# Kernel tuning notes

Hardware: AMD Instinct MI355X
Metric: run time of the kernel (lower is better)

Reference implementation:

```python
import jax, jax.numpy as jnp
import numpy as np

B, S, HID = 4, 4096, 1024
NUM_HEADS, HEAD_DIM = 16, 64  # HID // NUM_HEADS
EPS = 1e-8  # torch F.cosine_similarity eps


def setup_inputs() -> dict:
    key = jax.random.key(0)
    ks = jax.random.split(key, 12)
    scale = 1.0 / np.sqrt(HID)
    d = {
        "query": jax.random.normal(ks[0], (B, S, HID), jnp.float32),
        "key": jax.random.normal(ks[1], (B, S, HID), jnp.float32),
        "value": jax.random.normal(ks[2], (B, S, HID), jnp.float32),
        "Wq": jax.random.normal(ks[3], (HID, HID), jnp.float32) * scale,
        "bq": jnp.zeros((HID,), jnp.float32),
        "Wk": jax.random.normal(ks[4], (HID, HID), jnp.float32) * scale,
        "bk": jnp.zeros((HID,), jnp.float32),
        "Wv": jax.random.normal(ks[5], (HID, HID), jnp.float32) * scale,
        "bv": jnp.zeros((HID,), jnp.float32),
        "Wo": jax.random.normal(ks[6], (HID, HID), jnp.float32) * scale,
        "bo": jnp.zeros((HID,), jnp.float32),
        "score_weights": jax.random.normal(ks[7], (3,), jnp.float32),
    }
    return d


def reference(query, key, value, Wq, bq, Wk, bk, Wv, bv, Wo, bo, score_weights):
    # Projections; NOTE: original reshapes to (B, S, H, D) and never transposes,
    # so all attention scores are over the HEADS axis (shape (B,S,H,H)).
    q = (query @ Wq + bq).reshape(B, S, NUM_HEADS, HEAD_DIM)
    k = (key @ Wk + bk).reshape(B, S, NUM_HEADS, HEAD_DIM)
    v = (value @ Wv + bv).reshape(B, S, NUM_HEADS, HEAD_DIM)

    # Shared inner products between heads at each (b, s): (B, S, H, H)
    qk = jnp.einsum('bsqd,bskd->bsqk', q, k)

    # 1) scaled dot product
    dot = qk / jnp.sqrt(jnp.float32(HEAD_DIM))

    # 2) cosine similarity (F.cosine_similarity with eps=1e-8)
    qn = jnp.linalg.norm(q, axis=-1)  # (B,S,H)
    kn = jnp.linalg.norm(k, axis=-1)
    cos = qk / jnp.maximum(qn[..., :, None] * kn[..., None, :], EPS)

    # 3) negative Euclidean distance (torch.cdist, p=2)
    sq = jnp.sum(q * q, axis=-1)  # (B,S,H)
    sk = jnp.sum(k * k, axis=-1)
    dist2 = jnp.maximum(sq[..., :, None] + sk[..., None, :] - 2.0 * qk, 0.0)
    dist = -jnp.sqrt(dist2)

    w = jax.nn.softmax(score_weights)
    scores = w[0] * dot + w[1] * cos + w[2] * dist  # (B,S,H,H)

    attention = jax.nn.softmax(scores, axis=-1)  # dropout = identity (eval)
    out = jnp.einsum('bsqk,bskd->bsqd', attention, v)  # (B,S,H,D)

    # Faithful to torch: transpose(1,2) -> (B,H,S,D), then view (B, S, HID)
    out = out.transpose(0, 2, 1, 3).reshape(B, S, HID)
    return out @ Wo + bo, attention
```

## Files before the change

### kernel.cpp

```cpp
#include <hip/hip_runtime.h>
#include <stdint.h>

#define BB 4
#define SS 4096
#define HID 1024
#define NH 16
#define HD 64
#define TOKENS (BB * SS)

typedef unsigned short u16;
typedef __bf16 bf16x8 __attribute__((ext_vector_type(8)));
typedef float f32x4 __attribute__((ext_vector_type(4)));
typedef __attribute__((address_space(1))) unsigned int u32g;
typedef __attribute__((address_space(3))) unsigned int u32l;

__device__ __forceinline__ u16 f2bf(float f) {
  union { float f; unsigned u; } v; v.f = f;
  unsigned u = v.u;
  unsigned r = u + 0x7fffu + ((u >> 16) & 1u);
  return (u16)(r >> 16);
}
__device__ __forceinline__ float bf2f(u16 h) {
  union { unsigned u; float f; } v; v.u = ((unsigned)h) << 16;
  return v.f;
}

__device__ __forceinline__ void async16(const void* g, void* l) {
  __builtin_amdgcn_global_load_lds((const u32g*)g, (u32l*)l, 16, 0, 0);
}

__global__ __launch_bounds__(256) void transpose_cast(
    const float* __restrict__ W, u16* __restrict__ Wt) {
  __shared__ float t[32][33];
  const int bx = blockIdx.x * 32;
  const int by = blockIdx.y * 32;
  const int x = threadIdx.x;
#pragma unroll
  for (int yy = threadIdx.y; yy < 32; yy += 8)
    t[yy][x] = W[(size_t)(by + yy) * HID + bx + x];
  __syncthreads();
#pragma unroll
  for (int yy = threadIdx.y; yy < 32; yy += 8)
    Wt[(size_t)(bx + yy) * HID + by + x] = f2bf(t[x][yy]);
}

template <bool A_BF16, bool C_BF16>
__global__ __launch_bounds__(256, 2) void gemm_bt(
    const void* __restrict__ Av, const u16* __restrict__ Bt,
    const float* __restrict__ bias, void* __restrict__ Cv, int M, int N, int K) {
  __shared__ u16 As[128 * 32];
  __shared__ u16 Bs[128 * 32];
  const int tid = threadIdx.x;
  const int wave = tid >> 6, lane = tid & 63;
  const int quad = lane >> 4, l16 = lane & 15;
  const int m0 = blockIdx.y * 128, n0 = blockIdx.x * 128;
  const int wm = (wave >> 1) * 64, wn = (wave & 1) * 64;

  f32x4 acc[4][4] = {};

  for (int kt = 0; kt < K; kt += 32) {
    __syncthreads();
    {
      const u16* src = Bt + (size_t)n0 * K + kt;
#pragma unroll
      for (int is = 0; is < 2; ++is) {
        int g = is * 256 + wave * 64 + lane;
        const u16* gp = src + (size_t)(g >> 2) * K + (g & 3) * 8;
        u16* lp = &Bs[(is * 256 + wave * 64) * 8];
        async16(gp, lp);
      }
    }
    if (A_BF16) {
      const u16* src = (const u16*)Av + (size_t)m0 * K + kt;
#pragma unroll
      for (int is = 0; is < 2; ++is) {
        int g = is * 256 + wave * 64 + lane;
        const u16* gp = src + (size_t)(g >> 2) * K + (g & 3) * 8;
        u16* lp = &As[(is * 256 + wave * 64) * 8];
        async16(gp, lp);
      }
    } else {
      const float* src = (const float*)Av + (size_t)m0 * K + kt;
#pragma unroll
      for (int c = 0; c < 4; ++c) {
        int g = c * 256 + tid;
        int row = g >> 3, col = (g & 7) * 4;
        float4 f = *(const float4*)(src + (size_t)row * K + col);
        ushort4 h;
        h.x = f2bf(f.x); h.y = f2bf(f.y); h.z = f2bf(f.z); h.w = f2bf(f.w);
        *(ushort4*)&As[row * 32 + col] = h;
      }
    }
    __syncthreads();
    bf16x8 af[4], bfr[4];
#pragma unroll
    for (int i = 0; i < 4; ++i)
      af[i] = *(const bf16x8*)&As[(wm + i * 16 + l16) * 32 + quad * 8];
#pragma unroll
    for (int j = 0; j < 4; ++j)
      bfr[j] = *(const bf16x8*)&Bs[(wn + j * 16 + l16) * 32 + quad * 8];
#pragma unroll
    for (int i = 0; i < 4; ++i)
#pragma unroll
      for (int j = 0; j < 4; ++j)
        acc[i][j] = __builtin_amdgcn_mfma_f32_16x16x32_bf16(af[i], bfr[j],
                                                            acc[i][j], 0, 0, 0);
  }

  const int cb = n0 + wn + l16;
#pragma unroll
  for (int i = 0; i < 4; ++i) {
    int rowb = m0 + wm + i * 16 + quad * 4;
#pragma unroll
    for (int j = 0; j < 4; ++j) {
      int col = cb + j * 16;
      float bv = bias[col];
#pragma unroll
      for (int r = 0; r < 4; ++r) {
        float v = acc[i][j][r] + bv;
        if (C_BF16)
          ((u16*)Cv)[(size_t)(rowb + r) * N + col] = f2bf(v);
        else
          ((float*)Cv)[(size_t)(rowb + r) * N + col] = v;
      }
    }
  }
}

__global__ __launch_bounds__(256, 4) void attention_kernel(
    const u16* __restrict__ qb, const u16* __restrict__ kb,
    const u16* __restrict__ vb, const float* __restrict__ sw,
    float* __restrict__ attn_out, u16* __restrict__ o) {
  __shared__ float qs[16][65], ks[16][65], vs[16][65];
  __shared__ float sq[16], sk[16], qn[16], kn[16];
  __shared__ float attn_s[16][17];
  const int tid = threadIdx.x;
  const int token = blockIdx.x;
  const size_t base = (size_t)token * HID;

  {
    int idx = tid * 4;
    int h = idx >> 6, d = idx & 63;
    ushort4 uq = *(const ushort4*)(qb + base + idx);
    ushort4 uk = *(const ushort4*)(kb + base + idx);
    ushort4 uv = *(const ushort4*)(vb + base + idx);
    qs[h][d] = bf2f(uq.x); qs[h][d + 1] = bf2f(uq.y);
    qs[h][d + 2] = bf2f(uq.z); qs[h][d + 3] = bf2f(uq.w);
    ks[h][d] = bf2f(uk.x); ks[h][d + 1] = bf2f(uk.y);
    ks[h][d + 2] = bf2f(uk.z); ks[h][d + 3] = bf2f(uk.w);
    vs[h][d] = bf2f(uv.x); vs[h][d + 1] = bf2f(uv.y);
    vs[h][d + 2] = bf2f(uv.z); vs[h][d + 3] = bf2f(uv.w);
  }
  __syncthreads();

  if (tid < 32) {
    int i = tid & 15;
    const float* row = (tid < 16) ? qs[i] : ks[i];
    float s = 0.f;
#pragma unroll
    for (int d = 0; d < 64; ++d) s += row[d] * row[d];
    if (tid < 16) { sq[i] = s; qn[i] = sqrtf(s); }
    else          { sk[i] = s; kn[i] = sqrtf(s); }
  }
  __syncthreads();

  float s0 = sw[0], s1 = sw[1], s2 = sw[2];
  float smx = fmaxf(s0, fmaxf(s1, s2));
  float e0 = expf(s0 - smx), e1 = expf(s1 - smx), e2 = expf(s2 - smx);
  float winv = 1.f / (e0 + e1 + e2);
  float w0 = e0 * winv, w1 = e1 * winv, w2 = e2 * winv;

  const int i = tid >> 4, j = tid & 15;
  float attn;
  {
    float dot = 0.f;
#pragma unroll
    for (int d = 0; d < 64; ++d) dot += qs[i][d] * ks[j][d];
    float sdot = dot * 0.125f;
    float cosv = dot / fmaxf(qn[i] * kn[j], 1e-8f);
    float d2 = fmaxf(sq[i] + sk[j] - 2.f * dot, 0.f);
    float dist = -sqrtf(d2);
    float score = w0 * sdot + w1 * cosv + w2 * dist;
    float mx = score;
#pragma unroll
    for (int off = 8; off; off >>= 1) mx = fmaxf(mx, __shfl_xor(mx, off, 16));
    float e = expf(score - mx);
    float sum = e;
#pragma unroll
    for (int off = 8; off; off >>= 1) sum += __shfl_xor(sum, off, 16);
    attn = e / sum;
  }
  attn_out[(size_t)token * 256 + tid] = attn;
  attn_s[i][j] = attn;
  __syncthreads();

  {
    int d0 = j * 4;
    float o0 = 0.f, o1 = 0.f, o2 = 0.f, o3 = 0.f;
#pragma unroll
    for (int jj = 0; jj < 16; ++jj) {
      float a = attn_s[i][jj];
      o0 += a * vs[jj][d0];
      o1 += a * vs[jj][d0 + 1];
      o2 += a * vs[jj][d0 + 2];
      o3 += a * vs[jj][d0 + 3];
    }
    int b = token >> 12, s = token & (SS - 1);
    size_t off = (size_t)b * (SS * HID) + (size_t)i * (SS * HD) +
                 (size_t)s * HD + d0;
    ushort4 h;
    h.x = f2bf(o0); h.y = f2bf(o1); h.z = f2bf(o2); h.w = f2bf(o3);
    *(ushort4*)(o + off) = h;
  }
}

extern "C" void kernel_launch(void* const* d_in, const int* in_sizes, int n_in,
                              void* d_out, int out_size, void* d_ws,
                              size_t ws_size, hipStream_t stream) {
  (void)in_sizes; (void)n_in; (void)out_size; (void)ws_size;
  const float* query = (const float*)d_in[0];
  const float* key_  = (const float*)d_in[1];
  const float* value = (const float*)d_in[2];
  const float* Wq = (const float*)d_in[3];
  const float* bq = (const float*)d_in[4];
  const float* Wk = (const float*)d_in[5];
  const float* bk = (const float*)d_in[6];
  const float* Wv = (const float*)d_in[7];
  const float* bv = (const float*)d_in[8];
  const float* Wo = (const float*)d_in[9];
  const float* bo = (const float*)d_in[10];
  const float* sw = (const float*)d_in[11];

  char* ws = (char*)d_ws;
  u16* Wqt = (u16*)ws; ws += (size_t)HID * HID * 2;
  u16* Wkt = (u16*)ws; ws += (size_t)HID * HID * 2;
  u16* Wvt = (u16*)ws; ws += (size_t)HID * HID * 2;
  u16* Wot = (u16*)ws; ws += (size_t)HID * HID * 2;
  u16* qb = (u16*)ws; ws += (size_t)TOKENS * HID * 2;
  u16* kb = (u16*)ws; ws += (size_t)TOKENS * HID * 2;
  u16* vb = (u16*)ws; ws += (size_t)TOKENS * HID * 2;
  u16* ob = (u16*)ws; ws += (size_t)TOKENS * HID * 2;

  float* out0 = (float*)d_out;
  float* attn_out = out0 + (size_t)TOKENS * HID;

  dim3 tb(32, 8);
  dim3 tg(32, 32);
  transpose_cast<<<tg, tb, 0, stream>>>(Wq, Wqt);
  transpose_cast<<<tg, tb, 0, stream>>>(Wk, Wkt);
  transpose_cast<<<tg, tb, 0, stream>>>(Wv, Wvt);
  transpose_cast<<<tg, tb, 0, stream>>>(Wo, Wot);

  dim3 gg(HID / 128, TOKENS / 128);
  gemm_bt<false, true><<<gg, 256, 0, stream>>>(query, Wqt, bq, qb, TOKENS, HID, HID);
  gemm_bt<false, true><<<gg, 256, 0, stream>>>(key_, Wkt, bk, kb, TOKENS, HID, HID);
  gemm_bt<false, true><<<gg, 256, 0, stream>>>(value, Wvt, bv, vb, TOKENS, HID, HID);

  attention_kernel<<<TOKENS, 256, 0, stream>>>(qb, kb, vb, sw, attn_out, ob);

  gemm_bt<true, false><<<gg, 256, 0, stream>>>(ob, Wot, bo, out0, TOKENS, HID, HID);
}
```

Baseline: 572.3 us.

## Pre-cast inputs to bf16, batch QKV GEMMs into one launch, merge weight transposes

```diff
diff --git a/kernel.cpp b/kernel.cpp
--- a/kernel.cpp
+++ b/kernel.cpp
@@ -29,8 +29,31 @@
   __builtin_amdgcn_global_load_lds((const u32g*)g, (u32l*)l, 16, 0, 0);
 }
 
-__global__ __launch_bounds__(256) void transpose_cast(
-    const float* __restrict__ W, u16* __restrict__ Wt) {
+__global__ __launch_bounds__(256) void cast3_bf16(
+    const float* __restrict__ q, const float* __restrict__ k,
+    const float* __restrict__ v, u16* __restrict__ qo, u16* __restrict__ ko,
+    u16* __restrict__ vo) {
+  const int z = blockIdx.z;
+  const float* s = (z == 0) ? q : (z == 1) ? k : v;
+  u16* d = (z == 0) ? qo : (z == 1) ? ko : vo;
+  size_t i = ((size_t)blockIdx.x * 256 + threadIdx.x) * 8;
+  float4 f0 = *(const float4*)(s + i);
+  float4 f1 = *(const float4*)(s + i + 4);
+  ushort4 h0, h1;
+  h0.x = f2bf(f0.x); h0.y = f2bf(f0.y); h0.z = f2bf(f0.z); h0.w = f2bf(f0.w);
+  h1.x = f2bf(f1.x); h1.y = f2bf(f1.y); h1.z = f2bf(f1.z); h1.w = f2bf(f1.w);
+  *(ushort4*)(d + i) = h0;
+  *(ushort4*)(d + i + 4) = h1;
+}
+
+__global__ __launch_bounds__(256) void transpose_cast4(
+    const float* __restrict__ W0, const float* __restrict__ W1,
+    const float* __restrict__ W2, const float* __restrict__ W3,
+    u16* __restrict__ T0, u16* __restrict__ T1, u16* __restrict__ T2,
+    u16* __restrict__ T3) {
+  const int z = blockIdx.z;
+  const float* W = (z == 0) ? W0 : (z == 1) ? W1 : (z == 2) ? W2 : W3;
+  u16* Wt = (z == 0) ? T0 : (z == 1) ? T1 : (z == 2) ? T2 : T3;
   __shared__ float t[32][33];
   const int bx = blockIdx.x * 32;
   const int by = blockIdx.y * 32;
@@ -44,16 +67,31 @@
     Wt[(size_t)(bx + yy) * HID + by + x] = f2bf(t[x][yy]);
 }
 
-template <bool A_BF16, bool C_BF16>
-__global__ __launch_bounds__(256, 2) void gemm_bt(
-    const void* __restrict__ Av, const u16* __restrict__ Bt,
-    const float* __restrict__ bias, void* __restrict__ Cv, int M, int N, int K) {
+template <bool C_BF16, int NZ>
+__global__ __launch_bounds__(256, 4) void gemm_bt(
+    const u16* __restrict__ A0, const u16* __restrict__ A1,
+    const u16* __restrict__ A2, const u16* __restrict__ B0,
+    const u16* __restrict__ B1, const u16* __restrict__ B2,
+    const float* __restrict__ bias0, const float* __restrict__ bias1,
+    const float* __restrict__ bias2, void* __restrict__ C0,
+    void* __restrict__ C1, void* __restrict__ C2, int M, int N, int K) {
+  const u16* A = A0;
+  const u16* Bt = B0;
+  const float* bias = bias0;
+  void* Cv = C0;
+  if (NZ > 1) {
+    int z = blockIdx.z;
+    A = (z == 0) ? A0 : (z == 1) ? A1 : A2;
+    Bt = (z == 0) ? B0 : (z == 1) ? B1 : B2;
+    bias = (z == 0) ? bias0 : (z == 1) ? bias1 : bias2;
+    Cv = (z == 0) ? C0 : (z == 1) ? C1 : C2;
+  }
   __shared__ u16 As[128 * 32];
   __shared__ u16 Bs[128 * 32];
   const int tid = threadIdx.x;
   const int wave = tid >> 6, lane = tid & 63;
   const int quad = lane >> 4, l16 = lane & 15;
-  const int m0 = blockIdx.y * 128, n0 = blockIdx.x * 128;
+  const int m0 = blockIdx.x * 128, n0 = blockIdx.y * 128;
   const int wm = (wave >> 1) * 64, wn = (wave & 1) * 64;
 
   f32x4 acc[4][4] = {};
@@ -61,34 +99,15 @@
   for (int kt = 0; kt < K; kt += 32) {
     __syncthreads();
     {
-      const u16* src = Bt + (size_t)n0 * K + kt;
+      const u16* srcB = Bt + (size_t)n0 * K + kt;
+      const u16* srcA = A + (size_t)m0 * K + kt;
 #pragma unroll
       for (int is = 0; is < 2; ++is) {
         int g = is * 256 + wave * 64 + lane;
-        const u16* gp = src + (size_t)(g >> 2) * K + (g & 3) * 8;
-        u16* lp = &Bs[(is * 256 + wave * 64) * 8];
-        async16(gp, lp);
-      }
-    }
-    if (A_BF16) {
-      const u16* src = (const u16*)Av + (size_t)m0 * K + kt;
-#pragma unroll
-      for (int is = 0; is < 2; ++is) {
-        int g = is * 256 + wave * 64 + lane;
-        const u16* gp = src + (size_t)(g >> 2) * K + (g & 3) * 8;
-        u16* lp = &As[(is * 256 + wave * 64) * 8];
-        async16(gp, lp);
-      }
-    } else {
-      const float* src = (const float*)Av + (size_t)m0 * K + kt;
-#pragma unroll
-      for (int c = 0; c < 4; ++c) {
-        int g = c * 256 + tid;
-        int row = g >> 3, col = (g & 7) * 4;
-        float4 f = *(const float4*)(src + (size_t)row * K + col);
-        ushort4 h;
-        h.x = f2bf(f.x); h.y = f2bf(f.y); h.z = f2bf(f.z); h.w = f2bf(f.w);
-        *(ushort4*)&As[row * 32 + col] = h;
+        const u16* gpB = srcB + (size_t)(g >> 2) * K + (g & 3) * 8;
+        const u16* gpA = srcA + (size_t)(g >> 2) * K + (g & 3) * 8;
+        async16(gpB, &Bs[(is * 256 + wave * 64) * 8]);
+        async16(gpA, &As[(is * 256 + wave * 64) * 8]);
       }
     }
     __syncthreads();
@@ -236,6 +255,9 @@
   u16* Wkt = (u16*)ws; ws += (size_t)HID * HID * 2;
   u16* Wvt = (u16*)ws; ws += (size_t)HID * HID * 2;
   u16* Wot = (u16*)ws; ws += (size_t)HID * HID * 2;
+  u16* qh = (u16*)ws; ws += (size_t)TOKENS * HID * 2;
+  u16* kh = (u16*)ws; ws += (size_t)TOKENS * HID * 2;
+  u16* vh = (u16*)ws; ws += (size_t)TOKENS * HID * 2;
   u16* qb = (u16*)ws; ws += (size_t)TOKENS * HID * 2;
   u16* kb = (u16*)ws; ws += (size_t)TOKENS * HID * 2;
   u16* vb = (u16*)ws; ws += (size_t)TOKENS * HID * 2;
@@ -244,19 +266,18 @@
   float* out0 = (float*)d_out;
   float* attn_out = out0 + (size_t)TOKENS * HID;
 
-  dim3 tb(32, 8);
-  dim3 tg(32, 32);
-  transpose_cast<<<tg, tb, 0, stream>>>(Wq, Wqt);
-  transpose_cast<<<tg, tb, 0, stream>>>(Wk, Wkt);
-  transpose_cast<<<tg, tb, 0, stream>>>(Wv, Wvt);
-  transpose_cast<<<tg, tb, 0, stream>>>(Wo, Wot);
-
-  dim3 gg(HID / 128, TOKENS / 128);
-  gemm_bt<false, true><<<gg, 256, 0, stream>>>(query, Wqt, bq, qb, TOKENS, HID, HID);
-  gemm_bt<false, true><<<gg, 256, 0, stream>>>(key_, Wkt, bk, kb, TOKENS, HID, HID);
-  gemm_bt<false, true><<<gg, 256, 0, stream>>>(value, Wvt, bv, vb, TOKENS, HID, HID);
+  transpose_cast4<<<dim3(32, 32, 4), dim3(32, 8), 0, stream>>>(
+      Wq, Wk, Wv, Wo, Wqt, Wkt, Wvt, Wot);
+
+  cast3_bf16<<<dim3(TOKENS * HID / (256 * 8), 1, 3), 256, 0, stream>>>(
+      query, key_, value, qh, kh, vh);
+
+  gemm_bt<true, 3><<<dim3(TOKENS / 128, HID / 128, 3), 256, 0, stream>>>(
+      qh, kh, vh, Wqt, Wkt, Wvt, bq, bk, bv, qb, kb, vb, TOKENS, HID, HID);
 
   attention_kernel<<<TOKENS, 256, 0, stream>>>(qb, kb, vb, sw, attn_out, ob);
 
-  gemm_bt<true, false><<<gg, 256, 0, stream>>>(ob, Wot, bo, out0, TOKENS, HID, HID);
-}
+  gemm_bt<false, 1><<<dim3(TOKENS / 128, HID / 128, 1), 256, 0, stream>>>(
+      ob, nullptr, nullptr, Wot, nullptr, nullptr, bo, nullptr, nullptr,
+      out0, nullptr, nullptr, TOKENS, HID, HID);
+}
```

Result: faster. 506.7 us (-11.5%).
